# Kernel optimization log

Hardware: AMD Instinct MI355X
Metric: run time of the kernel (lower is better)

## Reference

```python
import jax, jax.numpy as jnp
import numpy as np
import math

L = 6          # num_layers
D = 512        # hidden_dim
S = 2048       # seq_len
B = 8          # batch
ODIM = 1       # output_dim
SCALES = (24.0, 720.0)


def setup_inputs() -> dict:
    key = jax.random.key(0)
    ks = jax.random.split(key, 12)
    def n(k, shape, scale=0.02):
        return jax.random.normal(k, shape, dtype=jnp.float32) * scale
    return {
        "z": jax.random.normal(ks[0], (B, S, 1), dtype=jnp.float32),
        "c": jax.random.normal(ks[1], (B, S, 1), dtype=jnp.float32),
        "enc_w": n(ks[2], (D, 2)), "enc_b": jnp.zeros((D,), jnp.float32),
        "beta": jnp.ones((L, len(SCALES)), jnp.float32),
        "wq": n(ks[3], (L, D, D)), "bq": jnp.zeros((L, D), jnp.float32),
        "wk": n(ks[4], (L, D, D)), "bk": jnp.zeros((L, D), jnp.float32),
        "wv": n(ks[5], (L, D, D)), "bv": jnp.zeros((L, D), jnp.float32),
        "ln1_w": jnp.ones((L, D), jnp.float32), "ln1_b": jnp.zeros((L, D), jnp.float32),
        "ln2_w": jnp.ones((L, D), jnp.float32), "ln2_b": jnp.zeros((L, D), jnp.float32),
        "ff1_w": n(ks[6], (L, 4 * D, D)), "ff1_b": jnp.zeros((L, 4 * D), jnp.float32),
        "ff2_w": n(ks[7], (L, D, 4 * D)), "ff2_b": jnp.zeros((L, D), jnp.float32),
        "out_w": n(ks[8], (ODIM, D)), "out_b": jnp.zeros((ODIM,), jnp.float32),
    }


def _ln(x, w, b, eps=1e-5):
    m = jnp.mean(x, axis=-1, keepdims=True)
    v = jnp.var(x, axis=-1, keepdims=True)
    return (x - m) * jax.lax.rsqrt(v + eps) * w + b


def _posenc(seq_len, dim):
    pos = jnp.arange(seq_len, dtype=jnp.float32)[:, None]
    div = jnp.exp(jnp.arange(0, dim, 2, dtype=jnp.float32) * (-(math.log(10000.0) / dim)))
    pe = jnp.zeros((seq_len, dim), jnp.float32)
    pe = pe.at[:, 0::2].set(jnp.sin(pos * div))
    pe = pe.at[:, 1::2].set(jnp.cos(pos * div))
    return pe


def reference(z, c, enc_w, enc_b, beta, wq, bq, wk, bk, wv, bv,
              ln1_w, ln1_b, ln2_w, ln2_b, ff1_w, ff1_b, ff2_w, ff2_b,
              out_w, out_b):
    # SequenceEncoder: cat(z,c) -> Linear(2, D) -> + sinusoidal PE
    x = jnp.concatenate([z, c], axis=-1) @ enc_w.T + enc_b       # [B,S,D]
    seq_len, d = x.shape[1], x.shape[2]
    x = x + _posenc(seq_len, d)[None]
    sqrt_d = math.sqrt(d)

    idx = jnp.arange(seq_len, dtype=jnp.float32)
    dist = jnp.abs(idx[:, None] - idx[None, :])                  # [S,S]

    for l in range(L):
        # pre-norm with ln1 (applied twice in the original code - replicated)
        xn = _ln(x, ln1_w[l], ln1_b[l])
        Q = xn @ wq[l].T + bq[l]
        K = xn @ wk[l].T + bk[l]
        V = xn @ wv[l].T + bv[l]
        attn = jnp.einsum('bid,bjd->bij', Q, K) / sqrt_d          # [B,S,S]
        bias = beta[l, 0] * jnp.cos(2.0 * math.pi * dist / SCALES[0]) \
             + beta[l, 1] * jnp.cos(2.0 * math.pi * dist / SCALES[1])
        probs = jax.nn.softmax(attn + bias, axis=-1)
        att_out = jnp.einsum('bij,bjd->bid', probs, V)
        # original applies layer_norm_1 again to the residual sum
        x = _ln(x + att_out, ln1_w[l], ln1_b[l])
        xn2 = _ln(x, ln2_w[l], ln2_b[l])
        h = jax.nn.relu(xn2 @ ff1_w[l].T + ff1_b[l])
        x = x + h @ ff2_w[l].T + ff2_b[l]

    return x @ out_w.T + out_b                                    # [B,S,ODIM]
```

## Files before the change

### kernel.cpp

```cpp
#include <hip/hip_runtime.h>
#include <hip/hip_fp8.h>
#include <math.h>

#define BB 8
#define SS 2048
#define DD 512
#define LL 6
#define FFD 2048

typedef _Float16 half_t;
typedef __attribute__((ext_vector_type(8))) _Float16 half8;
typedef __attribute__((ext_vector_type(4))) float f32x4;

enum { EPI_NONE = 0, EPI_RELU = 2, EPI_RES = 3, EPI_ATTN = 4, EPI_QKV = 5, EPI_PV = 6 };

__device__ __forceinline__ unsigned char f2e4m3(float v) {
    __hip_fp8_e4m3 f(v);
    return f.__x;
}

__device__ __forceinline__ void gl_lds16(const void* g, void* l) {
    __builtin_amdgcn_global_load_lds(
        (const __attribute__((address_space(1))) unsigned int*)g,
        (__attribute__((address_space(3))) unsigned int*)l,
        16, 0, 0);
}

__device__ __forceinline__ void blockReduce2(float& a, float& b, float* sm) {
#pragma unroll
    for (int off = 32; off; off >>= 1) {
        a += __shfl_down(a, off);
        b += __shfl_down(b, off);
    }
    int lane = threadIdx.x & 63;
    int w = threadIdx.x >> 6;
    if (lane == 0) { sm[w] = a; sm[4 + w] = b; }
    __syncthreads();
    a = sm[0] + sm[1] + sm[2] + sm[3];
    b = sm[4] + sm[5] + sm[6] + sm[7];
    __syncthreads();
}

__global__ __launch_bounds__(256) void encode_kernel(
    const float* __restrict__ z, const float* __restrict__ c,
    const float* __restrict__ enc_w, const float* __restrict__ enc_b,
    float* __restrict__ x)
{
    int idx = blockIdx.x * 256 + threadIdx.x;
    int d  = idx & (DD - 1);
    int bs = idx >> 9;
    int s  = bs & (SS - 1);
    float v = z[bs] * enc_w[2 * d] + c[bs] * enc_w[2 * d + 1] + enc_b[d];
    float div = expf(-(float)(d & ~1) * (9.210340371976184f / 512.0f));
    float ang = (float)s * div;
    v += (d & 1) ? cosf(ang) : sinf(ang);
    x[idx] = v;
}

__global__ __launch_bounds__(256) void convert_layer_kernel(
    const float* __restrict__ wq, const float* __restrict__ wk,
    const float* __restrict__ wv, const float* __restrict__ f1,
    const float* __restrict__ f2, half_t* __restrict__ wqkv,
    half_t* __restrict__ f1h, half_t* __restrict__ f2h)
{
    const int NQ = DD * DD;
    int i = blockIdx.x * 256 + threadIdx.x;
    if (i < 3 * NQ) {
        int which = i >> 18, j = i & (NQ - 1);
        const float* s = (which == 0) ? wq : (which == 1) ? wk : wv;
        wqkv[i] = (half_t)s[j];
    } else {
        int k = i - 3 * NQ;
        if (k < FFD * DD) f1h[k] = (half_t)f1[k];
        else              f2h[k - FFD * DD] = (half_t)f2[k - FFD * DD];
    }
}

__global__ __launch_bounds__(256) void bias_table_kernel(
    const float* __restrict__ beta, float* __restrict__ tbl)
{
    int i = blockIdx.x * 256 + threadIdx.x;
    int l = i >> 11, d = i & (SS - 1);
    tbl[i] = beta[2 * l] * cosf(0.2617993877991494f * d)
           + beta[2 * l + 1] * cosf(0.008726646259971648f * d);
}

__global__ __launch_bounds__(256) void ln_kernel(
    const float* __restrict__ src, const float* __restrict__ w,
    const float* __restrict__ b, half_t* __restrict__ dst)
{
    __shared__ float sm[8];
    size_t row = blockIdx.x;
    const float* p = src + row * DD;
    int t = threadIdx.x;
    float v0 = p[t], v1 = p[t + 256];
    float s = v0 + v1, sq = v0 * v0 + v1 * v1;
    blockReduce2(s, sq, sm);
    float mean = s * (1.0f / DD);
    float var  = sq * (1.0f / DD) - mean * mean;
    float rs   = rsqrtf(var + 1e-5f);
    dst[row * DD + t]       = (half_t)((v0 - mean) * rs * w[t] + b[t]);
    dst[row * DD + t + 256] = (half_t)((v1 - mean) * rs * w[t + 256] + b[t + 256]);
}

__global__ __launch_bounds__(256) void ln_ln_kernel(
    float* __restrict__ x,
    const float* __restrict__ w1, const float* __restrict__ b1,
    const float* __restrict__ w2, const float* __restrict__ b2,
    half_t* __restrict__ xn)
{
    __shared__ float sm[8];
    size_t row = blockIdx.x;
    int t = threadIdx.x;
    float v0 = x[row * DD + t];
    float v1 = x[row * DD + t + 256];
    float s = v0 + v1, sq = v0 * v0 + v1 * v1;
    blockReduce2(s, sq, sm);
    float mean = s * (1.0f / DD);
    float var  = sq * (1.0f / DD) - mean * mean;
    float rs   = rsqrtf(var + 1e-5f);
    float y0 = (v0 - mean) * rs * w1[t] + b1[t];
    float y1 = (v1 - mean) * rs * w1[t + 256] + b1[t + 256];
    x[row * DD + t]       = y0;
    x[row * DD + t + 256] = y1;
    s = y0 + y1; sq = y0 * y0 + y1 * y1;
    blockReduce2(s, sq, sm);
    mean = s * (1.0f / DD);
    var  = sq * (1.0f / DD) - mean * mean;
    rs   = rsqrtf(var + 1e-5f);
    xn[row * DD + t]       = (half_t)((y0 - mean) * rs * w2[t] + b2[t]);
    xn[row * DD + t + 256] = (half_t)((y1 - mean) * rs * w2[t + 256] + b2[t + 256]);
}

template<typename TIN, int BN, int EPI, int SWZ = 0>
__global__ __launch_bounds__(512) void gemm256(
    const void* __restrict__ Ap, const void* __restrict__ Wp,
    const float* __restrict__ bias, void* __restrict__ Cp,
    int N, int K, float alpha,
    long long sA, long long sW, long long sC,
    const float* __restrict__ biasK, const float* __restrict__ biasV,
    unsigned char* __restrict__ Ck, unsigned char* __restrict__ Cv)
{
    constexpr int ES  = (int)sizeof(TIN);
    constexpr int TN  = BN / 64;
    constexpr int ASZ = 256 * 128;
    constexpr int BSZ = BN * 128;
    constexpr int VM  = 4 + TN;
    constexpr int PHS = (TN == 4) ? ((ES == 2) ? 4 : 8) : ((ES == 2) ? 2 : 4);
    __shared__ __align__(16) unsigned char As[2 * ASZ];
    __shared__ __align__(16) unsigned char Bs[2 * BSZ];

    int bxi, byi, bzi;
    if (SWZ == 1) {
        const int id = blockIdx.x;
        const int ss2 = (id & 7) * 64 + (id >> 3);
        bxi = ss2 & 7; byi = (ss2 >> 3) & 7; bzi = ss2 >> 6;
    } else { bxi = blockIdx.x; byi = blockIdx.y; bzi = blockIdx.z; }

    const int z = bzi;
    const unsigned char* A = (const unsigned char*)Ap + (size_t)z * sA * ES;
    const unsigned char* W = (const unsigned char*)Wp + (size_t)z * sW * ES;
    float*  Cf = (float*)Cp  + (size_t)z * sC;
    half_t* Ch = (half_t*)Cp + (size_t)z * sC;
    unsigned char* C8 = (unsigned char*)Cp + (size_t)z * sC;

    const int tid = threadIdx.x;
    const int wv = tid >> 6, ln = tid & 63;
    const int bm = bxi * 256, bn = byi * BN;
    const int wm = (wv & 1) * 128, wn = (wv >> 1) * (BN / 4);

    const int srow  = tid >> 3;
    const int scolB = ((tid & 7) ^ ((tid >> 3) & 7)) * 16;
    const unsigned char* Ag = A + (size_t)(bm + srow) * K * ES + scolB;
    const unsigned char* Bg = W + (size_t)(bn + srow) * K * ES + scolB;

    f32x4 acc[8][TN] = {};
    f32x4 accd[8] = {};
    const long ONES8 = 0x3838383838383838L;

    const int lane15 = ln & 15, quad = ln >> 4;
    const int sw = lane15 & 7;
    const int nIter = (K * ES) / 128;

    auto stageCall = [&](int b, int t, int c) {
        const size_t ko = (size_t)t * 128;
        if (c < 4)
            gl_lds16(Ag + (size_t)(c * 64) * K * ES + ko,
                     As + b * ASZ + c * 8192 + wv * 1024);
        else {
            const int cb = c - 4;
            gl_lds16(Bg + (size_t)(cb * 64) * K * ES + ko,
                     Bs + b * BSZ + cb * 8192 + wv * 1024);
        }
    };

#pragma unroll
    for (int c = 0; c < VM; ++c) stageCall(0, 0, c);

    for (int it = 0; it < nIter; ++it) {
        const int cur = it & 1;
        asm volatile("s_waitcnt vmcnt(0)" ::: "memory");
        __builtin_amdgcn_s_barrier();

        const unsigned char* Ab = As + cur * ASZ;
        const unsigned char* Bb = Bs + cur * BSZ;
        const bool pf = (it + 1 < nIter);

        if constexpr (ES == 2 && TN == 4) {
#pragma unroll
            for (int ks = 0; ks < 2; ++ks) {
                half8 bF[4];
#pragma unroll
                for (int mq = 0; mq < 2; ++mq) {
                    const int cB = ((ks * 4 + quad) ^ sw) * 16;
                    half8 aF[4];
#pragma unroll
                    for (int i = 0; i < 4; ++i)
                        aF[i] = *(const half8*)(Ab + (wm + (mq * 4 + i) * 16 + lane15) * 128 + cB);
                    if (mq == 0)
#pragma unroll
                        for (int j = 0; j < 4; ++j)
                            bF[j] = *(const half8*)(Bb + (wn + j * 16 + lane15) * 128 + cB);
                    const int p = ks * 2 + mq;
                    if (pf)
#pragma unroll
                        for (int c = p * VM / PHS; c < (p + 1) * VM / PHS; ++c)
                            stageCall(cur ^ 1, it + 1, c);
                    __builtin_amdgcn_s_barrier();
                    asm volatile("s_waitcnt lgkmcnt(0)" ::: "memory");
                    __builtin_amdgcn_sched_barrier(0);
                    __builtin_amdgcn_s_setprio(1);
#pragma unroll
                    for (int i = 0; i < 4; ++i)
#pragma unroll
                        for (int j = 0; j < 4; ++j)
                            acc[mq * 4 + i][j] = __builtin_amdgcn_mfma_f32_16x16x32_f16(
                                aF[i], bF[j], acc[mq * 4 + i][j], 0, 0, 0);
                    __builtin_amdgcn_s_setprio(0);
                }
            }
        } else if constexpr (ES == 2 && TN == 2) {
#pragma unroll
            for (int ks = 0; ks < 2; ++ks) {
                const int cB = ((ks * 4 + quad) ^ sw) * 16;
                half8 aF[8], bF[2];
#pragma unroll
                for (int i = 0; i < 8; ++i)
                    aF[i] = *(const half8*)(Ab + (wm + i * 16 + lane15) * 128 + cB);
#pragma unroll
                for (int j = 0; j < 2; ++j)
                    bF[j] = *(const half8*)(Bb + (wn + j * 16 + lane15) * 128 + cB);
                const int p = ks;
                if (pf)
#pragma unroll
                    for (int c = p * VM / PHS; c < (p + 1) * VM / PHS; ++c)
                        stageCall(cur ^ 1, it + 1, c);
                __builtin_amdgcn_s_barrier();
                asm volatile("s_waitcnt lgkmcnt(0)" ::: "memory");
                __builtin_amdgcn_sched_barrier(0);
                __builtin_amdgcn_s_setprio(1);
#pragma unroll
                for (int i = 0; i < 8; ++i)
#pragma unroll
                    for (int j = 0; j < 2; ++j)
                        acc[i][j] = __builtin_amdgcn_mfma_f32_16x16x32_f16(
                            aF[i], bF[j], acc[i][j], 0, 0, 0);
                __builtin_amdgcn_s_setprio(0);
            }
        } else if constexpr (ES == 1 && TN == 4) {
#pragma unroll
            for (int ks = 0; ks < 4; ++ks) {
                long bF8[4];
#pragma unroll
                for (int mq = 0; mq < 2; ++mq) {
                    const int cB = (((ks * 2 + (quad >> 1)) ^ sw) * 16) + (quad & 1) * 8;
                    long aF8[4];
#pragma unroll
                    for (int i = 0; i < 4; ++i)
                        aF8[i] = *(const long*)(Ab + (wm + (mq * 4 + i) * 16 + lane15) * 128 + cB);
                    if (mq == 0)
#pragma unroll
                        for (int j = 0; j < 4; ++j)
                            bF8[j] = *(const long*)(Bb + (wn + j * 16 + lane15) * 128 + cB);
                    const int p = ks * 2 + mq;
                    if (pf)
#pragma unroll
                        for (int c = p * VM / PHS; c < (p + 1) * VM / PHS; ++c)
                            stageCall(cur ^ 1, it + 1, c);
                    __builtin_amdgcn_s_barrier();
                    asm volatile("s_waitcnt lgkmcnt(0)" ::: "memory");
                    __builtin_amdgcn_sched_barrier(0);
                    __builtin_amdgcn_s_setprio(1);
#pragma unroll
                    for (int i = 0; i < 4; ++i)
#pragma unroll
                        for (int j = 0; j < 4; ++j)
                            acc[mq * 4 + i][j] = __builtin_amdgcn_mfma_f32_16x16x32_fp8_fp8(
                                aF8[i], bF8[j], acc[mq * 4 + i][j], 0, 0, 0);
                    __builtin_amdgcn_s_setprio(0);
                }
            }
        } else {
#pragma unroll
            for (int ks = 0; ks < 4; ++ks) {
                const int cB = (((ks * 2 + (quad >> 1)) ^ sw) * 16) + (quad & 1) * 8;
                long aF8[8], bF8[2];
#pragma unroll
                for (int i = 0; i < 8; ++i)
                    aF8[i] = *(const long*)(Ab + (wm + i * 16 + lane15) * 128 + cB);
#pragma unroll
                for (int j = 0; j < 2; ++j)
                    bF8[j] = *(const long*)(Bb + (wn + j * 16 + lane15) * 128 + cB);
                const int p = ks;
                if (pf)
#pragma unroll
                    for (int c = p * VM / PHS; c < (p + 1) * VM / PHS; ++c)
                        stageCall(cur ^ 1, it + 1, c);
                __builtin_amdgcn_s_barrier();
                asm volatile("s_waitcnt lgkmcnt(0)" ::: "memory");
                __builtin_amdgcn_sched_barrier(0);
                __builtin_amdgcn_s_setprio(1);
#pragma unroll
                for (int i = 0; i < 8; ++i) {
#pragma unroll
                    for (int j = 0; j < 2; ++j)
                        acc[i][j] = __builtin_amdgcn_mfma_f32_16x16x32_fp8_fp8(
                            aF8[i], bF8[j], acc[i][j], 0, 0, 0);
                    if (EPI == EPI_PV)
                        accd[i] = __builtin_amdgcn_mfma_f32_16x16x32_fp8_fp8(
                            aF8[i], ONES8, accd[i], 0, 0, 0);
                }
                __builtin_amdgcn_s_setprio(0);
            }
        }
    }

    float invd[8][4];
    if (EPI == EPI_PV) {
#pragma unroll
        for (int i = 0; i < 8; ++i)
#pragma unroll
            for (int r = 0; r < 4; ++r)
                invd[i][r] = 1.0f / accd[i][r];
    }

#pragma unroll
    for (int i = 0; i < 8; ++i) {
        const int m0 = bm + wm + i * 16 + quad * 4;
#pragma unroll
        for (int j = 0; j < TN; ++j) {
            const int gn = bn + wn + j * 16 + lane15;
            if (EPI == EPI_QKV) {
                const int seg = gn >> 9, nn = gn & (DD - 1);
                if (seg == 2) {
                    unsigned int pk = 0;
#pragma unroll
                    for (int r = 0; r < 4; ++r)
                        pk |= (unsigned int)f2e4m3(acc[i][j][r] + biasV[nn]) << (8 * r);
                    const int b = m0 >> 11, s0 = m0 & (SS - 1);
                    *(unsigned int*)&Cv[((size_t)b * DD + nn) * SS + s0] = pk;
                } else {
                    const float bs = (seg == 0) ? bias[nn] : biasK[nn];
                    unsigned char* dst = (seg == 0) ? C8 : Ck;
#pragma unroll
                    for (int r = 0; r < 4; ++r)
                        dst[(size_t)(m0 + r) * DD + nn] = f2e4m3(acc[i][j][r] + bs);
                }
            } else {
#pragma unroll
                for (int r = 0; r < 4; ++r) {
                    const int gm = m0 + r;
                    float v = acc[i][j][r];
                    if (EPI == EPI_ATTN) {
                        int dist = gm - gn; if (dist < 0) dist = -dist;
                        v = __expf(fminf(v * alpha + bias[dist], 6.0f));
                        C8[(size_t)gm * N + gn] = f2e4m3(v);
                    } else if (EPI == EPI_PV) {
                        const size_t idx = (size_t)gm * N + gn;
                        Cf[idx] = v * invd[i][r] + Cf[idx];
                    } else if (EPI == EPI_RELU) {
                        Ch[(size_t)gm * N + gn] = (half_t)fmaxf(v + bias[gn], 0.0f);
                    } else {
                        const size_t idx = (size_t)gm * N + gn;
                        Cf[idx] = v + bias[gn] + Cf[idx];
                    }
                }
            }
        }
    }
}

__global__ __launch_bounds__(256) void out_kernel(
    const float* __restrict__ x, const float* __restrict__ ow,
    const float* __restrict__ ob, float* __restrict__ out)
{
    int row = blockIdx.x * 4 + (threadIdx.x >> 6);
    int lane = threadIdx.x & 63;
    const float* p = x + (size_t)row * DD;
    float s = 0.f;
#pragma unroll
    for (int k = 0; k < 8; ++k) s += p[lane + 64 * k] * ow[lane + 64 * k];
#pragma unroll
    for (int off = 32; off; off >>= 1) s += __shfl_down(s, off);
    if (lane == 0) out[row] = s + ob[0];
}

extern "C" void kernel_launch(void* const* d_in, const int* in_sizes, int n_in,
                              void* d_out, int out_size, void* d_ws, size_t ws_size,
                              hipStream_t stream)
{
    (void)in_sizes; (void)n_in; (void)out_size; (void)ws_size;
    const float* z     = (const float*)d_in[0];
    const float* c     = (const float*)d_in[1];
    const float* enc_w = (const float*)d_in[2];
    const float* enc_b = (const float*)d_in[3];
    const float* beta  = (const float*)d_in[4];
    const float* wq    = (const float*)d_in[5];
    const float* bq    = (const float*)d_in[6];
    const float* wk    = (const float*)d_in[7];
    const float* bk    = (const float*)d_in[8];
    const float* wv    = (const float*)d_in[9];
    const float* bv    = (const float*)d_in[10];
    const float* ln1w  = (const float*)d_in[11];
    const float* ln1b  = (const float*)d_in[12];
    const float* ln2w  = (const float*)d_in[13];
    const float* ln2b  = (const float*)d_in[14];
    const float* ff1w  = (const float*)d_in[15];
    const float* ff1b  = (const float*)d_in[16];
    const float* ff2w  = (const float*)d_in[17];
    const float* ff2b  = (const float*)d_in[18];
    const float* ow    = (const float*)d_in[19];
    const float* ob    = (const float*)d_in[20];

    const size_t BSD = (size_t)BB * SS * DD;
    const size_t BSS = (size_t)BB * SS * SS;

    char* p = (char*)d_ws;
    float*  x    = (float*)p;  p += BSD * 4;
    half_t* xnh  = (half_t*)p; p += BSD * 2;
    unsigned char* sch = (unsigned char*)p; p += BSS;
    unsigned char* qh  = (unsigned char*)p; p += BSD;
    unsigned char* kh  = (unsigned char*)p; p += BSD;
    unsigned char* vth = (unsigned char*)p; p += BSD;
    half_t* hh   = (half_t*)p; p += (size_t)BB * SS * FFD * 2;
    half_t* wqkv = (half_t*)p; p += (size_t)3 * DD * DD * 2;
    half_t* f1h  = (half_t*)p; p += (size_t)FFD * DD * 2;
    half_t* f2h  = (half_t*)p; p += (size_t)FFD * DD * 2;
    float*  tbl  = (float*)p;

    const float alpha = 0.044194173824159216f;
    const int BS = BB * SS;
    const long long sQ = (long long)SS * DD, sP = (long long)SS * SS,
                    sV = (long long)DD * SS;
    const int CONV_BLKS = (3 * DD * DD + 2 * FFD * DD) / 256;

    bias_table_kernel<<<LL * SS / 256, 256, 0, stream>>>(beta, tbl);
    encode_kernel<<<BS * DD / 256, 256, 0, stream>>>(z, c, enc_w, enc_b, x);

    for (int l = 0; l < LL; ++l) {
        convert_layer_kernel<<<CONV_BLKS, 256, 0, stream>>>(
            wq + (size_t)l * DD * DD, wk + (size_t)l * DD * DD,
            wv + (size_t)l * DD * DD, ff1w + (size_t)l * FFD * DD,
            ff2w + (size_t)l * DD * FFD, wqkv, f1h, f2h);

        ln_kernel<<<BS, 256, 0, stream>>>(x, ln1w + l * DD, ln1b + l * DD, xnh);

        gemm256<half_t, 128, EPI_QKV><<<dim3(BS / 256, 12, 1), 512, 0, stream>>>(
            xnh, wqkv, bq + l * DD, qh, 1536, DD, 0, 0, 0, 0,
            bk + l * DD, bv + l * DD, kh, vth);

        gemm256<unsigned char, 256, EPI_ATTN, 1><<<dim3(512, 1, 1), 512, 0, stream>>>(
            qh, kh, tbl + l * SS, sch, SS, DD, alpha, sQ, sQ, sP,
            nullptr, nullptr, nullptr, nullptr);

        gemm256<unsigned char, 128, EPI_PV><<<dim3(SS / 256, DD / 128, BB), 512, 0, stream>>>(
            sch, vth, nullptr, x, DD, SS, 0, sP, sV, sQ,
            nullptr, nullptr, nullptr, nullptr);

        ln_ln_kernel<<<BS, 256, 0, stream>>>(x, ln1w + l * DD, ln1b + l * DD,
                                             ln2w + l * DD, ln2b + l * DD, xnh);

        gemm256<half_t, 256, EPI_RELU><<<dim3(BS / 256, FFD / 256, 1), 512, 0, stream>>>(
            xnh, f1h, ff1b + l * FFD, hh, FFD, DD, 0, 0, 0, 0,
            nullptr, nullptr, nullptr, nullptr);
        gemm256<half_t, 128, EPI_RES><<<dim3(BS / 256, DD / 128, 1), 512, 0, stream>>>(
            hh, f2h, ff2b + l * DD, x, DD, FFD, 0, 0, 0, 0,
            nullptr, nullptr, nullptr, nullptr);
    }

    out_kernel<<<BS / 4, 256, 0, stream>>>(x, ow, ob, (float*)d_out);
}
```

Baseline: 1.796 ms.

## Triple-buffer LDS stages in BN=128 GEMM with partial vmcnt waits

For the BN=128 GEMM variants, LDS staging grows from two to three buffers and loads are issued two iterations ahead. The wait at each iteration only blocks until the oldest stage has landed (vmcnt(VM)) rather than draining all outstanding loads. This is meant to hide more global-to-LDS latency behind MFMA work. In exchange it uses 50% more LDS, which may reduce occupancy, and it relies on the vmcnt count matching the per-iteration load count exactly.

```diff
diff --git a/kernel.cpp b/kernel.cpp
--- a/kernel.cpp
+++ b/kernel.cpp
@@ -24,6 +24,13 @@
         (const __attribute__((address_space(1))) unsigned int*)g,
         (__attribute__((address_space(3))) unsigned int*)l,
         16, 0, 0);
+}
+
+template<int N> __device__ __forceinline__ void waitcnt_vm() {
+    if constexpr (N == 0)      asm volatile("s_waitcnt vmcnt(0)" ::: "memory");
+    else if constexpr (N == 6) asm volatile("s_waitcnt vmcnt(6)" ::: "memory");
+    else if constexpr (N == 8) asm volatile("s_waitcnt vmcnt(8)" ::: "memory");
+    else                       asm volatile("s_waitcnt vmcnt(0)" ::: "memory");
 }
 
 __device__ __forceinline__ void blockReduce2(float& a, float& b, float* sm) {
@@ -147,8 +154,9 @@
     constexpr int BSZ = BN * 128;
     constexpr int VM  = 4 + TN;
     constexpr int PHS = (TN == 4) ? ((ES == 2) ? 4 : 8) : ((ES == 2) ? 2 : 4);
-    __shared__ __align__(16) unsigned char As[2 * ASZ];
-    __shared__ __align__(16) unsigned char Bs[2 * BSZ];
+    constexpr int NB  = (BN == 128) ? 3 : 2;
+    __shared__ __align__(16) unsigned char As[NB * ASZ];
+    __shared__ __align__(16) unsigned char Bs[NB * BSZ];
 
     int bxi, byi, bzi;
     if (SWZ == 1) {
@@ -196,15 +204,29 @@
 
 #pragma unroll
     for (int c = 0; c < VM; ++c) stageCall(0, 0, c);
+    if constexpr (NB == 3) {
+        if (nIter > 1) {
+#pragma unroll
+            for (int c = 0; c < VM; ++c) stageCall(1, 1, c);
+        }
+    }
 
     for (int it = 0; it < nIter; ++it) {
-        const int cur = it & 1;
-        asm volatile("s_waitcnt vmcnt(0)" ::: "memory");
+        if constexpr (NB == 3) {
+            if (it + 1 < nIter) waitcnt_vm<VM>();
+            else               waitcnt_vm<0>();
+        } else {
+            waitcnt_vm<0>();
+        }
         __builtin_amdgcn_s_barrier();
+
+        const int cur  = (NB == 3) ? (it % 3) : (it & 1);
+        const int stg  = (NB == 3) ? ((it + 2) % 3) : (cur ^ 1);
+        const int stgT = (NB == 3) ? (it + 2) : (it + 1);
+        const bool pf  = stgT < nIter;
 
         const unsigned char* Ab = As + cur * ASZ;
         const unsigned char* Bb = Bs + cur * BSZ;
-        const bool pf = (it + 1 < nIter);
 
         if constexpr (ES == 2 && TN == 4) {
 #pragma unroll
@@ -225,7 +247,7 @@
                     if (pf)
 #pragma unroll
                         for (int c = p * VM / PHS; c < (p + 1) * VM / PHS; ++c)
-                            stageCall(cur ^ 1, it + 1, c);
+                            stageCall(stg, stgT, c);
                     __builtin_amdgcn_s_barrier();
                     asm volatile("s_waitcnt lgkmcnt(0)" ::: "memory");
                     __builtin_amdgcn_sched_barrier(0);
@@ -254,7 +276,7 @@
                 if (pf)
 #pragma unroll
                     for (int c = p * VM / PHS; c < (p + 1) * VM / PHS; ++c)
-                        stageCall(cur ^ 1, it + 1, c);
+                        stageCall(stg, stgT, c);
                 __builtin_amdgcn_s_barrier();
                 asm volatile("s_waitcnt lgkmcnt(0)" ::: "memory");
                 __builtin_amdgcn_sched_barrier(0);
@@ -286,7 +308,7 @@
                     if (pf)
 #pragma unroll
                         for (int c = p * VM / PHS; c < (p + 1) * VM / PHS; ++c)
-                            stageCall(cur ^ 1, it + 1, c);
+                            stageCall(stg, stgT, c);
                     __builtin_amdgcn_s_barrier();
                     asm volatile("s_waitcnt lgkmcnt(0)" ::: "memory");
                     __builtin_amdgcn_sched_barrier(0);
@@ -315,7 +337,7 @@
                 if (pf)
 #pragma unroll
                     for (int c = p * VM / PHS; c < (p + 1) * VM / PHS; ++c)
-                        stageCall(cur ^ 1, it + 1, c);
+                        stageCall(stg, stgT, c);
                 __builtin_amdgcn_s_barrier();
                 asm volatile("s_waitcnt lgkmcnt(0)" ::: "memory");
                 __builtin_amdgcn_sched_barrier(0);
```

Measured after the change: 1.901 ms. 1.06x slower.
